# Kernel tuning notes

Measured on AMD Instinct MI355X. Metric: run time of the kernel, lower is better.

## Reference

```python
import jax, jax.numpy as jnp
import numpy as np

N_NODES = 10000
N_EDGES = 320000
HIDDEN = 128
MIX = 8


def setup_inputs() -> dict:
    key = jax.random.key(0)
    k1, k2, k3, k4 = jax.random.split(key, 4)
    X = jax.random.normal(k1, (N_NODES, HIDDEN), dtype=jnp.float32)
    # nn.Linear default init scale ~ 1/sqrt(fan_in)
    W_A = jax.random.normal(k2, (HIDDEN, HIDDEN), dtype=jnp.float32) / np.sqrt(HIDDEN)
    W_B = jax.random.normal(k3, (MIX, HIDDEN), dtype=jnp.float32) / np.sqrt(HIDDEN)
    edge_index = jax.random.randint(k4, (2, N_EDGES), 0, N_NODES, dtype=jnp.int64)
    return {"X": X, "W_A": W_A, "W_B": W_B, "edge_index": edge_index, "num_nodes": N_NODES}


def reference(X, W_A, W_B, edge_index, num_nodes):
    src, dst = edge_index[0], edge_index[1]
    X_src = X[src]                                            # (E, h) gather
    # hyper-network weights per edge: W_B(gelu(W_A(x)))  -> (E, mix)
    W_tar_edge = jax.nn.gelu(X_src @ W_A.T, approximate=False) @ W_B.T
    # edge-wise outer product (E, h, mix)
    cross = X_src[:, :, None] * W_tar_edge[:, None, :]
    # scatter-add into node bins (N, h, mix)
    agg = jnp.zeros((num_nodes, X.shape[1], W_tar_edge.shape[1]), dtype=X.dtype)
    agg = agg.at[dst].add(cross)
    agg = jax.nn.gelu(agg, approximate=False)
    # gather back per edge and contract over mix dim -> (E, h)
    out_edge = jnp.einsum('ehm,em->eh', agg[dst], W_tar_edge)
    return (out_edge, src, dst)
```

## Files before the change

kernel.cpp:

```cpp
#include <hip/hip_runtime.h>

#define HIDDEN 128
#define MIX 8
#define CAP 128

#define NBW 32
#define LDX 33
#define KT  16
#define LDW 17
#define LDG 132

typedef float v2f __attribute__((ext_vector_type(2)));

__device__ __forceinline__ float gelu_exact(float x) {
    return 0.5f * x * (1.0f + erff(x * 0.7071067811865476f));
}

__global__ __launch_bounds__(256) void k_prep(const float* __restrict__ X,
                                              const float* __restrict__ W_A,
                                              const float* __restrict__ W_B,
                                              float* __restrict__ Wnode,
                                              const int* __restrict__ src,
                                              const int* __restrict__ dst,
                                              int* __restrict__ cursor,
                                              int2* __restrict__ bins,
                                              float* __restrict__ out_src,
                                              float* __restrict__ out_dst,
                                              int N, int E, int WB) {
    int t = threadIdx.x;

    if ((int)blockIdx.x >= WB) {
        int e = ((int)blockIdx.x - WB) * 256 + t;
        if (e < E) {
            int d = dst[e];
            int s = src[e];
            int p = atomicAdd(&cursor[d], 1);
            if (p < CAP) bins[(size_t)d * CAP + p] = make_int2(e, s);
            __builtin_nontemporal_store((float)s, &out_src[e]);
            __builtin_nontemporal_store((float)d, &out_dst[e]);
        }
        return;
    }

    __shared__ union SmemU {
        struct { float xs[NBW * LDX]; float wa[HIDDEN * LDW]; } ab;
        float gsm[NBW * LDG];
    } u;
    __shared__ float wb[MIX * LDG];

    int n0 = blockIdx.x * NBW;

    {
        int r = t >> 3;
        int c0 = (t & 7) * 16;
        int rn = n0 + r; if (rn >= N) rn = N - 1;
        const float* xp = X + (size_t)rn * HIDDEN + c0;
        float4 a = ((const float4*)xp)[0];
        float4 bb = ((const float4*)xp)[1];
        float4 c = ((const float4*)xp)[2];
        float4 d = ((const float4*)xp)[3];
        float tmp[16] = {a.x,a.y,a.z,a.w, bb.x,bb.y,bb.z,bb.w,
                         c.x,c.y,c.z,c.w, d.x,d.y,d.z,d.w};
#pragma unroll
        for (int q = 0; q < 16; ++q) u.ab.xs[r * LDX + c0 + q] = tmp[q];
    }

    int ngrp = t & 7;
    int jgrp = t >> 3;
    float acc[4][4];
#pragma unroll
    for (int i = 0; i < 4; ++i)
#pragma unroll
        for (int j = 0; j < 4; ++j) acc[i][j] = 0.f;

    for (int kt = 0; kt < HIDDEN; kt += KT) {
        __syncthreads();
        {
            int j = t >> 1;
            int c0 = (t & 1) * 8;
            const float* wp = W_A + (size_t)j * HIDDEN + kt + c0;
            float4 a = ((const float4*)wp)[0];
            float4 bb = ((const float4*)wp)[1];
            float tmp[8] = {a.x,a.y,a.z,a.w, bb.x,bb.y,bb.z,bb.w};
#pragma unroll
            for (int q = 0; q < 8; ++q) u.ab.wa[j * LDW + c0 + q] = tmp[q];
        }
        __syncthreads();
#pragma unroll
        for (int k = 0; k < KT; ++k) {
            float xv[4], wv[4];
#pragma unroll
            for (int i = 0; i < 4; ++i) xv[i] = u.ab.xs[(ngrp * 4 + i) * LDX + kt + k];
#pragma unroll
            for (int j = 0; j < 4; ++j) wv[j] = u.ab.wa[(jgrp * 4 + j) * LDW + k];
#pragma unroll
            for (int i = 0; i < 4; ++i)
#pragma unroll
                for (int j = 0; j < 4; ++j) acc[i][j] += xv[i] * wv[j];
        }
    }
    __syncthreads();

#pragma unroll
    for (int i = 0; i < 4; ++i)
#pragma unroll
        for (int j = 0; j < 4; ++j)
            u.gsm[(ngrp * 4 + i) * LDG + (jgrp * 4 + j)] = gelu_exact(acc[i][j]);

    if (t < 64) {
        int r = t >> 3;
        int c0 = (t & 7) * 16;
        const float* wp = W_B + (size_t)r * HIDDEN + c0;
        float4 a = ((const float4*)wp)[0];
        float4 bb = ((const float4*)wp)[1];
        float4 c = ((const float4*)wp)[2];
        float4 d = ((const float4*)wp)[3];
        float tmp[16] = {a.x,a.y,a.z,a.w, bb.x,bb.y,bb.z,bb.w,
                         c.x,c.y,c.z,c.w, d.x,d.y,d.z,d.w};
#pragma unroll
        for (int q = 0; q < 16; ++q) wb[r * LDG + c0 + q] = tmp[q];
    }
    __syncthreads();

    {
        int n = t >> 3;
        int m = t & 7;
        float a = 0.f;
#pragma unroll 8
        for (int k = 0; k < HIDDEN; ++k)
            a += u.gsm[n * LDG + k] * wb[m * LDG + k];
        if (n0 + n < N) Wnode[(size_t)n0 * MIX + t] = a;
    }
}

__global__ __launch_bounds__(256) void k_node(const float* __restrict__ X,
                                              const float* __restrict__ Wnode,
                                              const int2* __restrict__ bins,
                                              const int* __restrict__ cursor,
                                              float* __restrict__ out_edge,
                                              int N) {
    __shared__ __align__(16) float wsm[4 * 64 * 8];
    int t = threadIdx.x;
    int lane = t & 63;
    float* ws = wsm + (t >> 6) * (64 * 8);

    int n = blockIdx.x * 4 + (t >> 6);
    if (n >= N) return;
    int cnt = cursor[n];
    if (cnt > CAP) cnt = CAP;
    if (cnt == 0) return;
    const int2* bp = bins + (size_t)n * CAP;

    float ag0[MIX], ag1[MIX];
#pragma unroll
    for (int m = 0; m < MIX; ++m) { ag0[m] = 0.f; ag1[m] = 0.f; }

    for (int c0 = 0; c0 < cnt; c0 += 64) {
        int nb = min(64, cnt - c0);
        int idx = c0 + ((lane < nb) ? lane : 0);
        int2 es = bp[idx];
        int s_l = es.y;
        {
            const float4* wv = (const float4*)(Wnode + (size_t)s_l * MIX);
            float4 wlo = wv[0];
            float4 whi = wv[1];
            float4* wd = (float4*)(ws + (lane << 3));
            wd[0] = wlo; wd[1] = whi;
        }
#pragma unroll 8
        for (int i = 0; i < nb; ++i) {
            int s = __builtin_amdgcn_readlane(s_l, i);
            float2 x = ((const float2*)(X + (size_t)s * HIDDEN))[lane];
            const float4* wr = (const float4*)(ws + (i << 3));
            float4 w0 = wr[0];
            float4 w1 = wr[1];
            ag0[0] += x.x * w0.x; ag0[1] += x.x * w0.y;
            ag0[2] += x.x * w0.z; ag0[3] += x.x * w0.w;
            ag0[4] += x.x * w1.x; ag0[5] += x.x * w1.y;
            ag0[6] += x.x * w1.z; ag0[7] += x.x * w1.w;
            ag1[0] += x.y * w0.x; ag1[1] += x.y * w0.y;
            ag1[2] += x.y * w0.z; ag1[3] += x.y * w0.w;
            ag1[4] += x.y * w1.x; ag1[5] += x.y * w1.y;
            ag1[6] += x.y * w1.z; ag1[7] += x.y * w1.w;
        }
    }

#pragma unroll
    for (int m = 0; m < MIX; ++m) {
        ag0[m] = gelu_exact(ag0[m]);
        ag1[m] = gelu_exact(ag1[m]);
    }

    for (int c0 = 0; c0 < cnt; c0 += 64) {
        int nb = min(64, cnt - c0);
        int idx = c0 + ((lane < nb) ? lane : 0);
        int2 es = bp[idx];
        int e_l = es.x, s_l = es.y;
        {
            const float4* wv = (const float4*)(Wnode + (size_t)s_l * MIX);
            float4 wlo = wv[0];
            float4 whi = wv[1];
            float4* wd = (float4*)(ws + (lane << 3));
            wd[0] = wlo; wd[1] = whi;
        }
#pragma unroll 4
        for (int i = 0; i < nb; ++i) {
            int e = __builtin_amdgcn_readlane(e_l, i);
            const float4* wr = (const float4*)(ws + (i << 3));
            float4 w0 = wr[0];
            float4 w1 = wr[1];
            v2f o;
            o.x = ag0[0]*w0.x + ag0[1]*w0.y + ag0[2]*w0.z + ag0[3]*w0.w
                + ag0[4]*w1.x + ag0[5]*w1.y + ag0[6]*w1.z + ag0[7]*w1.w;
            o.y = ag1[0]*w0.x + ag1[1]*w0.y + ag1[2]*w0.z + ag1[3]*w0.w
                + ag1[4]*w1.x + ag1[5]*w1.y + ag1[6]*w1.z + ag1[7]*w1.w;
            __builtin_nontemporal_store(o, (v2f*)(out_edge + (size_t)e * HIDDEN) + lane);
        }
    }
}

extern "C" void kernel_launch(void* const* d_in, const int* in_sizes, int n_in,
                              void* d_out, int out_size, void* d_ws, size_t ws_size,
                              hipStream_t stream) {
    const float* X   = (const float*)d_in[0];
    const float* W_A = (const float*)d_in[1];
    const float* W_B = (const float*)d_in[2];
    const int*   ei  = (const int*)d_in[3];

    const int N = in_sizes[0] / HIDDEN;
    const int E = in_sizes[3] / 2;
    const int* src = ei;
    const int* dst = ei + E;

    float* out      = (float*)d_out;
    float* out_edge = out;
    float* out_src  = out + (size_t)E * HIDDEN;
    float* out_dst  = out_src + E;

    int*  cursor = (int*)d_ws;
    int2* bins   = (int2*)(cursor + N);
    float* Wnode = (float*)(bins + (size_t)N * CAP);

    hipMemsetAsync(cursor, 0, sizeof(int) * (size_t)N, stream);

    int WB = (N + NBW - 1) / NBW;
    int EB = (E + 255) / 256;

    k_prep<<<WB + EB, 256, 0, stream>>>(X, W_A, W_B, Wnode, src, dst,
                                        cursor, bins, out_src, out_dst, N, E, WB);
    k_node<<<(N + 3) / 4, 256, 0, stream>>>(X, Wnode, bins, cursor, out_edge, N);
}
```

Measured before the change: 250.0 us.

## Split wavefront into half-waves processing two edges per iteration with float4 accesses

```diff
diff --git a/kernel.cpp b/kernel.cpp
--- a/kernel.cpp
+++ b/kernel.cpp
@@ -10,6 +10,7 @@
 #define LDW 17
 #define LDG 132
 
+typedef float v4f __attribute__((ext_vector_type(4)));
 typedef float v2f __attribute__((ext_vector_type(2)));
 
 __device__ __forceinline__ float gelu_exact(float x) {
@@ -139,10 +140,12 @@
                                               const int* __restrict__ cursor,
                                               float* __restrict__ out_edge,
                                               int N) {
-    __shared__ __align__(16) float wsm[4 * 64 * 8];
+    __shared__ __align__(16) float wsm[4][64 * 8];
     int t = threadIdx.x;
     int lane = t & 63;
-    float* ws = wsm + (t >> 6) * (64 * 8);
+    int half = lane >> 5;
+    int hq = lane & 31;
+    float* ws = wsm[t >> 6];
 
     int n = blockIdx.x * 4 + (t >> 6);
     if (n >= N) return;
@@ -151,70 +154,94 @@
     if (cnt == 0) return;
     const int2* bp = bins + (size_t)n * CAP;
 
-    float ag0[MIX], ag1[MIX];
-#pragma unroll
-    for (int m = 0; m < MIX; ++m) { ag0[m] = 0.f; ag1[m] = 0.f; }
+    int slot = 2 * hq + half;
+
+    v4f ag[MIX];
+#pragma unroll
+    for (int m = 0; m < MIX; ++m) ag[m] = 0.f;
 
     for (int c0 = 0; c0 < cnt; c0 += 64) {
         int nb = min(64, cnt - c0);
-        int idx = c0 + ((lane < nb) ? lane : 0);
+        int idx = c0 + ((slot < nb) ? slot : 0);
         int2 es = bp[idx];
         int s_l = es.y;
         {
-            const float4* wv = (const float4*)(Wnode + (size_t)s_l * MIX);
-            float4 wlo = wv[0];
-            float4 whi = wv[1];
-            float4* wd = (float4*)(ws + (lane << 3));
+            const v4f* wv = (const v4f*)(Wnode + (size_t)s_l * MIX);
+            v4f wlo = wv[0], whi = wv[1];
+            v4f* wd = (v4f*)(ws + (slot << 3));
             wd[0] = wlo; wd[1] = whi;
         }
-#pragma unroll 8
-        for (int i = 0; i < nb; ++i) {
-            int s = __builtin_amdgcn_readlane(s_l, i);
-            float2 x = ((const float2*)(X + (size_t)s * HIDDEN))[lane];
-            const float4* wr = (const float4*)(ws + (i << 3));
-            float4 w0 = wr[0];
-            float4 w1 = wr[1];
-            ag0[0] += x.x * w0.x; ag0[1] += x.x * w0.y;
-            ag0[2] += x.x * w0.z; ag0[3] += x.x * w0.w;
-            ag0[4] += x.x * w1.x; ag0[5] += x.x * w1.y;
-            ag0[6] += x.x * w1.z; ag0[7] += x.x * w1.w;
-            ag1[0] += x.y * w0.x; ag1[1] += x.y * w0.y;
-            ag1[2] += x.y * w0.z; ag1[3] += x.y * w0.w;
-            ag1[4] += x.y * w1.x; ag1[5] += x.y * w1.y;
-            ag1[6] += x.y * w1.z; ag1[7] += x.y * w1.w;
+        int npair = nb >> 1;
+#pragma unroll 4
+        for (int p = 0; p < npair; ++p) {
+            int s = __shfl(s_l, p + (half << 5), 64);
+            v4f x = ((const v4f*)(X + (size_t)s * HIDDEN))[hq];
+            const v4f* wr = (const v4f*)(ws + (((p << 1) | half) << 3));
+            v4f w0 = wr[0], w1 = wr[1];
+            ag[0] += x * w0.x; ag[1] += x * w0.y;
+            ag[2] += x * w0.z; ag[3] += x * w0.w;
+            ag[4] += x * w1.x; ag[5] += x * w1.y;
+            ag[6] += x * w1.z; ag[7] += x * w1.w;
+        }
+        if (nb & 1) {
+            int j = nb - 1;
+            int s = __shfl(s_l, ((j & 1) << 5) + (j >> 1), 64);
+            v4f x = half ? (v4f)0.f : ((const v4f*)(X + (size_t)s * HIDDEN))[hq];
+            const v4f* wr = (const v4f*)(ws + (j << 3));
+            v4f w0 = wr[0], w1 = wr[1];
+            ag[0] += x * w0.x; ag[1] += x * w0.y;
+            ag[2] += x * w0.z; ag[3] += x * w0.w;
+            ag[4] += x * w1.x; ag[5] += x * w1.y;
+            ag[6] += x * w1.z; ag[7] += x * w1.w;
         }
     }
 
 #pragma unroll
     for (int m = 0; m < MIX; ++m) {
-        ag0[m] = gelu_exact(ag0[m]);
-        ag1[m] = gelu_exact(ag1[m]);
-    }
-
+        ag[m].x += __shfl_xor(ag[m].x, 32, 64);
+        ag[m].y += __shfl_xor(ag[m].y, 32, 64);
+        ag[m].z += __shfl_xor(ag[m].z, 32, 64);
+        ag[m].w += __shfl_xor(ag[m].w, 32, 64);
+    }
+#pragma unroll
+    for (int m = 0; m < MIX; ++m) {
+        ag[m].x = gelu_exact(ag[m].x);
+        ag[m].y = gelu_exact(ag[m].y);
+        ag[m].z = gelu_exact(ag[m].z);
+        ag[m].w = gelu_exact(ag[m].w);
+    }
+
+    bool restage = (cnt > 64);
     for (int c0 = 0; c0 < cnt; c0 += 64) {
         int nb = min(64, cnt - c0);
-        int idx = c0 + ((lane < nb) ? lane : 0);
+        int idx = c0 + ((slot < nb) ? slot : 0);
         int2 es = bp[idx];
-        int e_l = es.x, s_l = es.y;
-        {
-            const float4* wv = (const float4*)(Wnode + (size_t)s_l * MIX);
-            float4 wlo = wv[0];
-            float4 whi = wv[1];
-            float4* wd = (float4*)(ws + (lane << 3));
+        int e_l = es.x;
+        if (restage) {
+            const v4f* wv = (const v4f*)(Wnode + (size_t)es.y * MIX);
+            v4f wlo = wv[0], whi = wv[1];
+            v4f* wd = (v4f*)(ws + (slot << 3));
             wd[0] = wlo; wd[1] = whi;
         }
-#pragma unroll 4
-        for (int i = 0; i < nb; ++i) {
-            int e = __builtin_amdgcn_readlane(e_l, i);
-            const float4* wr = (const float4*)(ws + (i << 3));
-            float4 w0 = wr[0];
-            float4 w1 = wr[1];
-            v2f o;
-            o.x = ag0[0]*w0.x + ag0[1]*w0.y + ag0[2]*w0.z + ag0[3]*w0.w
-                + ag0[4]*w1.x + ag0[5]*w1.y + ag0[6]*w1.z + ag0[7]*w1.w;
-            o.y = ag1[0]*w0.x + ag1[1]*w0.y + ag1[2]*w0.z + ag1[3]*w0.w
-                + ag1[4]*w1.x + ag1[5]*w1.y + ag1[6]*w1.z + ag1[7]*w1.w;
-            __builtin_nontemporal_store(o, (v2f*)(out_edge + (size_t)e * HIDDEN) + lane);
+        int npair = nb >> 1;
+#pragma unroll 2
+        for (int p = 0; p < npair; ++p) {
+            int e = __shfl(e_l, p + (half << 5), 64);
+            const v4f* wr = (const v4f*)(ws + (((p << 1) | half) << 3));
+            v4f w0 = wr[0], w1 = wr[1];
+            v4f o = ag[0] * w0.x + ag[1] * w0.y + ag[2] * w0.z + ag[3] * w0.w
+                  + ag[4] * w1.x + ag[5] * w1.y + ag[6] * w1.z + ag[7] * w1.w;
+            __builtin_nontemporal_store(o, (v4f*)(out_edge + (size_t)e * HIDDEN) + hq);
+        }
+        if (nb & 1) {
+            int j = nb - 1;
+            int e = __shfl(e_l, ((j & 1) << 5) + (j >> 1), 64);
+            const v4f* wr = (const v4f*)(ws + (j << 3));
+            v4f w0 = wr[0], w1 = wr[1];
+            v4f o = ag[0] * w0.x + ag[1] * w0.y + ag[2] * w0.z + ag[3] * w0.w
+                  + ag[4] * w1.x + ag[5] * w1.y + ag[6] * w1.z + ag[7] * w1.w;
+            if (half == 0)
+                __builtin_nontemporal_store(o, (v4f*)(out_edge + (size_t)e * HIDDEN) + hq);
         }
     }
 }
```

After: 251.1 us. About the same (+0.4%).
